# Performance work log

Measured on AMD Instinct MI355X. Metric: run time of the kernel, lower is better.

## Reference

```python
import jax, jax.numpy as jnp
import numpy as np

B, L, E, H = 2, 1024, 1024, 16
D = E // H  # head_dim = 64
EPS = 1e-6


def setup_inputs() -> dict:
    key = jax.random.key(0)
    ks = jax.random.split(key, 6)
    x = jax.random.normal(ks[0], (B, L, E), dtype=jnp.float32)
    qkv_w = jax.random.normal(ks[1], (E, 3 * E), dtype=jnp.float32) / np.sqrt(E)
    qkv_b = jnp.zeros((3 * E,), dtype=jnp.float32)
    out_w = jax.random.normal(ks[2], (E, E), dtype=jnp.float32) / np.sqrt(E)
    out_b = jnp.zeros((E,), dtype=jnp.float32)
    norm1_w = jnp.ones((E,), dtype=jnp.float32)
    norm2_w = jnp.ones((E,), dtype=jnp.float32)
    mlp_w1 = jax.random.normal(ks[3], (E, 4 * E), dtype=jnp.float32) / np.sqrt(E)
    mlp_b1 = jnp.zeros((4 * E,), dtype=jnp.float32)
    mlp_w2 = jax.random.normal(ks[4], (4 * E, E), dtype=jnp.float32) / np.sqrt(4 * E)
    mlp_b2 = jnp.zeros((E,), dtype=jnp.float32)
    return dict(x=x, qkv_w=qkv_w, qkv_b=qkv_b, out_w=out_w, out_b=out_b,
                norm1_w=norm1_w, norm2_w=norm2_w,
                mlp_w1=mlp_w1, mlp_b1=mlp_b1, mlp_w2=mlp_w2, mlp_b2=mlp_b2)


def rmsnorm(x, w, eps=1e-6):
    var = jnp.mean(jnp.square(x), axis=-1, keepdims=True)
    return x * jax.lax.rsqrt(var + eps) * w


def cosformer_attn(x, qkv_w, qkv_b, out_w, out_b):
    b, l, e = x.shape
    qkv = x @ qkv_w + qkv_b
    q, k, v = jnp.split(qkv, 3, axis=-1)
    # [B, H, L, D]
    q = q.reshape(b, l, H, D).transpose(0, 2, 1, 3)
    k = k.reshape(b, l, H, D).transpose(0, 2, 1, 3)
    v = v.reshape(b, l, H, D).transpose(0, 2, 1, 3)
    positions = jnp.arange(l, dtype=jnp.float32).reshape(1, 1, l, 1)
    cos_w = jnp.cos(jnp.pi / 2 * positions / l)
    sin_w = jnp.sin(jnp.pi / 2 * positions / l)
    q_prime = jax.nn.relu(q)
    k_prime = jax.nn.relu(k)
    q_cos, q_sin = q_prime * cos_w, q_prime * sin_w
    k_cos, k_sin = k_prime * cos_w, k_prime * sin_w
    # running KV state: cumsum over L of per-position outer products [B,H,L,D,D]
    kv_cos_cumsum = jnp.cumsum(jnp.einsum('bhld,bhle->bhlde', k_cos, v), axis=2)
    context_cos = jnp.einsum('bhld,bhlde->bhle', q_cos, kv_cos_cumsum)
    kv_sin_cumsum = jnp.cumsum(jnp.einsum('bhld,bhle->bhlde', k_sin, v), axis=2)
    context_sin = jnp.einsum('bhld,bhlde->bhle', q_sin, kv_sin_cumsum)
    context = context_cos + context_sin
    k_cos_cumsum = jnp.cumsum(k_cos, axis=2)
    k_sin_cumsum = jnp.cumsum(k_sin, axis=2)
    norm = (jnp.einsum('bhld,bhld->bhl', q_cos, k_cos_cumsum)
            + jnp.einsum('bhld,bhld->bhl', q_sin, k_sin_cumsum))
    output = context / (norm[..., None] + EPS)
    output = output.transpose(0, 2, 1, 3).reshape(b, l, e)
    return output @ out_w + out_b


def reference(x, qkv_w, qkv_b, out_w, out_b, norm1_w, norm2_w,
              mlp_w1, mlp_b1, mlp_w2, mlp_b2):
    # pre-norm transformer block with cosformer causal linear attention
    h = x + cosformer_attn(rmsnorm(x, norm1_w), qkv_w, qkv_b, out_w, out_b)
    m = rmsnorm(h, norm2_w)
    m = jax.nn.gelu(m @ mlp_w1 + mlp_b1) @ mlp_w2 + mlp_b2
    return h + m
```

## Files before the change

### kernel.cpp

```cpp
#include <hip/hip_runtime.h>

#define TB_L 1024
#define TB_E 1024

typedef __attribute__((ext_vector_type(8))) short bf16x8;
typedef __attribute__((ext_vector_type(8))) unsigned short u16x8;
typedef __attribute__((ext_vector_type(4))) float floatx4;

#define AS1(p) ((const __attribute__((address_space(1))) void*)(p))
#define AS3(p) ((__attribute__((address_space(3))) void*)(p))

static __device__ __forceinline__ unsigned short f2bf(float x) {
  union { float f; unsigned u; } c; c.f = x;
  unsigned r = c.u + 0x7fff + ((c.u >> 16) & 1);
  return (unsigned short)(r >> 16);
}
static __device__ __forceinline__ float gelu_f(float x) {
  const float c0 = 0.7978845608028654f;
  const float c1 = 0.044715f;
  float x3 = x * x * x;
  return 0.5f * x * (1.0f + tanhf(c0 * (x + c1 * x3)));
}

static __device__ __forceinline__ int swz(int row, int bytecol) {
  return row * 128 +
         ((((bytecol >> 4) ^ ((row + (row >> 3)) & 7)) << 4) | (bytecol & 15));
}

__global__ __launch_bounds__(256) void rms_kernel(const float* __restrict__ x,
                                                  const float* __restrict__ w,
                                                  unsigned short* __restrict__ out) {
  const int row = blockIdx.x;
  const int tid = threadIdx.x;
  const float4 v = *(const float4*)(x + (size_t)row * TB_E + tid * 4);
  float s = v.x * v.x + v.y * v.y + v.z * v.z + v.w * v.w;
#pragma unroll
  for (int off = 32; off > 0; off >>= 1) s += __shfl_down(s, off);
  __shared__ float red[4];
  if ((tid & 63) == 0) red[tid >> 6] = s;
  __syncthreads();
  const float tot = red[0] + red[1] + red[2] + red[3];
  const float scale = rsqrtf(tot * (1.0f / TB_E) + 1e-6f);
  const float4 wv = *(const float4*)(w + tid * 4);
  ushort4 o;
  o.x = f2bf(v.x * scale * wv.x);
  o.y = f2bf(v.y * scale * wv.y);
  o.z = f2bf(v.z * scale * wv.z);
  o.w = f2bf(v.w * scale * wv.w);
  *(ushort4*)(out + (size_t)row * TB_E + tid * 4) = o;
}

__global__ __launch_bounds__(256) void transpose_all(
    const float* __restrict__ s0, const float* __restrict__ s1,
    const float* __restrict__ s2, const float* __restrict__ s3,
    unsigned short* __restrict__ d0, unsigned short* __restrict__ d1,
    unsigned short* __restrict__ d2, unsigned short* __restrict__ d3) {
  const int id = blockIdx.x;
  const float* in; unsigned short* out; int K, N, lid;
  if (id < 768)       { in = s0; out = d0; K = 1024; N = 3072; lid = id; }
  else if (id < 1024) { in = s1; out = d1; K = 1024; N = 1024; lid = id - 768; }
  else if (id < 2048) { in = s2; out = d2; K = 1024; N = 4096; lid = id - 1024; }
  else                { in = s3; out = d3; K = 4096; N = 1024; lid = id - 2048; }
  const int nx = N >> 6;
  const int n0 = (lid % nx) * 64, k0 = (lid / nx) * 64;
  __shared__ float t[64][65];
  const int tid = threadIdx.x;
#pragma unroll
  for (int rep = 0; rep < 4; ++rep) {
    const int r = rep * 16 + (tid >> 4);
    const int c = (tid & 15) * 4;
    const float4 v = *(const float4*)(in + (size_t)(k0 + r) * N + n0 + c);
    t[r][c] = v.x; t[r][c + 1] = v.y; t[r][c + 2] = v.z; t[r][c + 3] = v.w;
  }
  __syncthreads();
#pragma unroll
  for (int rep = 0; rep < 4; ++rep) {
    const int n = rep * 16 + (tid >> 4);
    const int k = (tid & 15) * 4;
    ushort4 o;
    o.x = f2bf(t[k + 0][n]);
    o.y = f2bf(t[k + 1][n]);
    o.z = f2bf(t[k + 2][n]);
    o.w = f2bf(t[k + 3][n]);
    *(ushort4*)(out + (size_t)(n0 + n) * K + k0 + k) = o;
  }
}

template <int BM, int BN, int WM, int WN, bool GELU>
__global__ __launch_bounds__(256) void gemm_bf16(
    const unsigned short* __restrict__ A, const unsigned short* __restrict__ Bt,
    const float* __restrict__ bias, const float* __restrict__ res,
    float* __restrict__ Cf, unsigned short* __restrict__ Cb,
    float* __restrict__ Cpart, int M, int N, int K, int Ksl) {
  constexpr int WCOLS = BN / WN;
  constexpr int MT = WM / 16;
  constexpr int NT = WN / 16;
  constexpr int ACH = BM / 16;
  constexpr int BCH = BN / 16;
  static_assert((BM / WM) * (BN / WN) == 4, "4 waves");
  static_assert(ACH % 4 == 0 && BCH % 4 == 0, "chunks divisible by waves");
  __shared__ __align__(16) unsigned short As[2][BM * 32];
  __shared__ __align__(16) unsigned short Bs[2][BN * 32];
  const int tid = threadIdx.x;
  const int wid = tid >> 6, lane = tid & 63;
  const int m0 = blockIdx.y * BM, n0 = blockIdx.x * BN;
  const int k_off = blockIdx.z * Ksl;
  const int mbase = (wid / WCOLS) * WM, nbase = (wid % WCOLS) * WN;

  floatx4 acc[MT][NT];
#pragma unroll
  for (int i = 0; i < MT; ++i)
#pragma unroll
    for (int j = 0; j < NT; ++j) {
      floatx4 z = {0.f, 0.f, 0.f, 0.f};
      acc[i][j] = z;
    }

  const int srow = lane >> 2;
  const int scol = (lane & 3) * 8;
  const unsigned short* Ag = A + (size_t)m0 * K + k_off;
  const unsigned short* Bg = Bt + (size_t)n0 * K + k_off;
  const int fr = (lane & 15);
  const int fk = (lane >> 4) * 16;

  auto stage = [&](int buf, int k0) {
#pragma unroll
    for (int j = 0; j < ACH / 4; ++j) {
      const int ch = j * 4 + wid;
      __builtin_amdgcn_global_load_lds(
          AS1(Ag + (size_t)(ch * 16 + srow) * K + k0 + scol),
          AS3((char*)&As[buf][0] + ch * 1024), 16, 0, 0);
    }
#pragma unroll
    for (int j = 0; j < BCH / 4; ++j) {
      const int ch = j * 4 + wid;
      __builtin_amdgcn_global_load_lds(
          AS1(Bg + (size_t)(ch * 16 + srow) * K + k0 + scol),
          AS3((char*)&Bs[buf][0] + ch * 1024), 16, 0, 0);
    }
  };

  stage(0, 0);
  const int nsteps = Ksl / 32;
  for (int s = 0; s < nsteps; ++s) {
    __syncthreads();
    const int cur = s & 1;
    if (s + 1 < nsteps) stage(cur ^ 1, (s + 1) * 32);
    const char* Ab = (const char*)&As[cur][0];
    const char* Bb = (const char*)&Bs[cur][0];
    bf16x8 af[MT], bfr[NT];
#pragma unroll
    for (int i = 0; i < MT; ++i)
      af[i] = *(const bf16x8*)(Ab + (mbase / 16 + i) * 1024 + fr * 64 + fk);
#pragma unroll
    for (int j = 0; j < NT; ++j)
      bfr[j] = *(const bf16x8*)(Bb + (nbase / 16 + j) * 1024 + fr * 64 + fk);
#pragma unroll
    for (int i = 0; i < MT; ++i)
#pragma unroll
      for (int j = 0; j < NT; ++j)
        acc[i][j] = __builtin_amdgcn_mfma_f32_16x16x32_bf16(af[i], bfr[j],
                                                            acc[i][j], 0, 0, 0);
  }

  const int mr = (lane >> 4) * 4;
  const int nc = lane & 15;
  float* P = Cpart ? (Cpart + (size_t)blockIdx.z * M * N) : nullptr;
#pragma unroll
  for (int i = 0; i < MT; ++i)
#pragma unroll
    for (int j = 0; j < NT; ++j) {
      const int n = n0 + nbase + j * 16 + nc;
      const float bv = bias ? bias[n] : 0.f;
#pragma unroll
      for (int r = 0; r < 4; ++r) {
        const int m = m0 + mbase + i * 16 + mr + r;
        float v = acc[i][j][r] + bv;
        if (GELU) v = gelu_f(v);
        if (res) v += res[(size_t)m * N + n];
        if (P) P[(size_t)m * N + n] = v;
        if (Cf) Cf[(size_t)m * N + n] = v;
        if (Cb) Cb[(size_t)m * N + n] = f2bf(v);
      }
    }
}

__global__ __launch_bounds__(256) void reduce_out(const float* __restrict__ P,
                                                  const float* __restrict__ h,
                                                  const float* __restrict__ b2,
                                                  float* __restrict__ out) {
  const int idx = (blockIdx.x * 256 + threadIdx.x) * 4;
  const int n = idx & 1023;
  const float4 a = *(const float4*)(P + idx);
  const float4 b = *(const float4*)(P + 2097152 + idx);
  const float4 hh = *(const float4*)(h + idx);
  const float4 bb = *(const float4*)(b2 + n);
  float4 o;
  o.x = a.x + b.x + hh.x + bb.x;
  o.y = a.y + b.y + hh.y + bb.y;
  o.z = a.z + b.z + hh.z + bb.z;
  o.w = a.w + b.w + hh.w + bb.w;
  *(float4*)(out + idx) = o;
}

__global__ __launch_bounds__(256) void attn_mfma(const unsigned short* __restrict__ qkv,
                                                 unsigned short* __restrict__ out) {
  const int it = blockIdx.x;
  const int bh = blockIdx.y;
  const int b = bh >> 4, h = bh & 15;
  const int tid = threadIdx.x;
  const int w = tid >> 6, lane = tid & 63;
  const int qd = lane >> 4, ln = lane & 15;
  const int i0 = it * 64;
  __shared__ __align__(16) char sq[8192];
  __shared__ __align__(16) char sk[8192];
  __shared__ __align__(16) char svt[8192];
  __shared__ __align__(16) char ss[8192];
  const unsigned short* base = qkv + (size_t)b * (TB_L * 3072) + h * 64;
  const float PH = 1.5339807878856412e-3f;

#pragma unroll
  for (int p = 0; p < 2; ++p) {
    const int flat = p * 256 + tid;
    const int r = flat >> 3, c = flat & 7;
    u16x8 v = *(const u16x8*)(base + (size_t)(i0 + r) * 3072 + c * 8);
#pragma unroll
    for (int z = 0; z < 8; ++z) v[z] = (v[z] & 0x8000) ? (unsigned short)0 : v[z];
    *(u16x8*)(sq + swz(r, c * 16)) = v;
  }
  __syncthreads();

  bf16x8 aq[2];
#pragma unroll
  for (int ks = 0; ks < 2; ++ks)
    aq[ks] = *(const bf16x8*)(sq + swz(w * 16 + ln, ks * 64 + qd * 16));

  float ci[4], si[4];
#pragma unroll
  for (int r = 0; r < 4; ++r)
    __sincosf(PH * (float)(i0 + w * 16 + qd * 4 + r), &si[r], &ci[r]);

  floatx4 acc_o[4], acc_n;
  {
    floatx4 z = {0.f, 0.f, 0.f, 0.f};
#pragma unroll
    for (int nt = 0; nt < 4; ++nt) acc_o[nt] = z;
    acc_n = z;
  }
  bf16x8 ones;
#pragma unroll
  for (int z = 0; z < 8; ++z) ones[z] = (short)0x3F80;

  for (int jt = 0; jt <= it; ++jt) {
    const int j0 = jt * 64;
    __syncthreads();
#pragma unroll
    for (int p = 0; p < 2; ++p) {
      const int flat = p * 256 + tid;
      const int r = flat >> 3, c = flat & 7;
      u16x8 kv = *(const u16x8*)(base + (size_t)(j0 + r) * 3072 + 1024 + c * 8);
#pragma unroll
      for (int z = 0; z < 8; ++z) kv[z] = (kv[z] & 0x8000) ? (unsigned short)0 : kv[z];
      *(u16x8*)(sk + swz(r, c * 16)) = kv;
      u16x8 vv = *(const u16x8*)(base + (size_t)(j0 + r) * 3072 + 2048 + c * 8);
#pragma unroll
      for (int z = 0; z < 8; ++z)
        *(unsigned short*)(svt + swz(c * 8 + z, r * 2)) = (unsigned short)vv[z];
    }
    __syncthreads();

    floatx4 s_acc[4];
    {
      floatx4 z = {0.f, 0.f, 0.f, 0.f};
#pragma unroll
      for (int nt = 0; nt < 4; ++nt) s_acc[nt] = z;
    }
#pragma unroll
    for (int ks = 0; ks < 2; ++ks)
#pragma unroll
      for (int nt = 0; nt < 4; ++nt) {
        const bf16x8 bk = *(const bf16x8*)(sk + swz(nt * 16 + ln, ks * 64 + qd * 16));
        s_acc[nt] = __builtin_amdgcn_mfma_f32_16x16x32_bf16(aq[ks], bk, s_acc[nt], 0, 0, 0);
      }

    float cj[4], sj[4];
#pragma unroll
    for (int nt = 0; nt < 4; ++nt)
      __sincosf(PH * (float)(j0 + nt * 16 + ln), &sj[nt], &cj[nt]);
    const bool diag = (jt == it);
    const int li = w * 16 + qd * 4;
#pragma unroll
    for (int nt = 0; nt < 4; ++nt) {
      const int jl = nt * 16 + ln;
#pragma unroll
      for (int r = 0; r < 4; ++r) {
        float val = s_acc[nt][r] * (ci[r] * cj[nt] + si[r] * sj[nt]);
        if (diag && jl > li + r) val = 0.f;
        *(unsigned short*)(ss + swz(li + r, jl * 2)) = f2bf(val);
      }
    }

#pragma unroll
    for (int ks = 0; ks < 2; ++ks) {
      const bf16x8 as = *(const bf16x8*)(ss + swz(w * 16 + ln, ks * 64 + qd * 16));
#pragma unroll
      for (int nt = 0; nt < 4; ++nt) {
        const bf16x8 bv = *(const bf16x8*)(svt + swz(nt * 16 + ln, ks * 64 + qd * 16));
        acc_o[nt] = __builtin_amdgcn_mfma_f32_16x16x32_bf16(as, bv, acc_o[nt], 0, 0, 0);
      }
      acc_n = __builtin_amdgcn_mfma_f32_16x16x32_bf16(as, ones, acc_n, 0, 0, 0);
    }
  }

#pragma unroll
  for (int r = 0; r < 4; ++r) {
    const float inv = 1.0f / (acc_n[r] + 1e-6f);
    unsigned short* op =
        out + (size_t)(b * TB_L + i0 + w * 16 + qd * 4 + r) * TB_E + h * 64;
#pragma unroll
    for (int nt = 0; nt < 4; ++nt) op[nt * 16 + ln] = f2bf(acc_o[nt][r] * inv);
  }
}

extern "C" void kernel_launch(void* const* d_in, const int* in_sizes, int n_in,
                              void* d_out, int out_size, void* d_ws, size_t ws_size,
                              hipStream_t stream) {
  const float* x     = (const float*)d_in[0];
  const float* qkv_w = (const float*)d_in[1];
  const float* qkv_b = (const float*)d_in[2];
  const float* out_w = (const float*)d_in[3];
  const float* out_b = (const float*)d_in[4];
  const float* n1w   = (const float*)d_in[5];
  const float* n2w   = (const float*)d_in[6];
  const float* w1    = (const float*)d_in[7];
  const float* b1    = (const float*)d_in[8];
  const float* w2    = (const float*)d_in[9];
  const float* b2    = (const float*)d_in[10];

  char* wsb = (char*)d_ws;
  unsigned short* qkvb  = (unsigned short*)wsb;
  unsigned short* g     = (unsigned short*)wsb;
  unsigned short* xnb   = (unsigned short*)(wsb + 16777216);
  unsigned short* attnb = (unsigned short*)(wsb + 20971520);
  float*          h     = (float*)(wsb + 25165824);
  unsigned short* qkvwt = (unsigned short*)(wsb + 33554432);
  unsigned short* outwt = (unsigned short*)(wsb + 39845888);
  unsigned short* w1t   = (unsigned short*)(wsb + 41943040);
  unsigned short* w2t   = (unsigned short*)(wsb + 50331648);
  float*          Pk    = (float*)(wsb + 33554432);
  float* out = (float*)d_out;
  const int M = 2048;

  transpose_all<<<dim3(3072), 256, 0, stream>>>(qkv_w, out_w, w1, w2,
                                                qkvwt, outwt, w1t, w2t);

  rms_kernel<<<dim3(M), 256, 0, stream>>>(x, n1w, xnb);
  gemm_bf16<64, 128, 32, 64, false><<<dim3(24, 32), 256, 0, stream>>>(
      xnb, qkvwt, qkv_b, nullptr, nullptr, qkvb, nullptr, M, 3072, 1024, 1024);
  attn_mfma<<<dim3(16, 32), 256, 0, stream>>>(qkvb, attnb);
  gemm_bf16<64, 64, 32, 32, false><<<dim3(16, 32), 256, 0, stream>>>(
      attnb, outwt, out_b, x, h, nullptr, nullptr, M, 1024, 1024, 1024);
  rms_kernel<<<dim3(M), 256, 0, stream>>>(h, n2w, xnb);
  gemm_bf16<64, 128, 32, 64, true><<<dim3(32, 32), 256, 0, stream>>>(
      xnb, w1t, b1, nullptr, nullptr, g, nullptr, M, 4096, 1024, 1024);
  gemm_bf16<64, 64, 32, 32, false><<<dim3(16, 32, 2), 256, 0, stream>>>(
      g, w2t, nullptr, nullptr, nullptr, nullptr, Pk, M, 1024, 4096, 2048);
  reduce_out<<<dim3(2048), 256, 0, stream>>>(Pk, h, b2, out);
}
```

Measured before the change: 279.0 us.

## Generalize GEMM to BK=64 and 8-wave blocks with grouped tile rasterization

Parameterizes the bf16 GEMM on K-tile depth and thread count, doubling K per stage to 64 so each barrier covers two MFMA k-chunks. The large GEMMs now use 512-thread blocks with 32x32 per-wave tiles, and the second MLP GEMM moves to 64x128 tiles. It also adds grouped block rasterization (groups of 4 M-tiles) to improve L2 reuse of the weight tiles. This doubles LDS use per block and changes the register and occupancy balance.

After: 264.8 us. -5.1%, faster.

```diff
diff --git a/kernel.cpp b/kernel.cpp
--- a/kernel.cpp
+++ b/kernel.cpp
@@ -86,24 +86,33 @@
   }
 }
 
-template <int BM, int BN, int WM, int WN, bool GELU>
-__global__ __launch_bounds__(256) void gemm_bf16(
+template <int BM, int BN, int BK, int WM, int WN, int NTH, bool GELU>
+__global__ __launch_bounds__(NTH) void gemm_bf16(
     const unsigned short* __restrict__ A, const unsigned short* __restrict__ Bt,
     const float* __restrict__ bias, const float* __restrict__ res,
     float* __restrict__ Cf, unsigned short* __restrict__ Cb,
     float* __restrict__ Cpart, int M, int N, int K, int Ksl) {
+  constexpr int NW = NTH / 64;
+  constexpr int KC = BK / 32;
   constexpr int WCOLS = BN / WN;
   constexpr int MT = WM / 16;
   constexpr int NT = WN / 16;
-  constexpr int ACH = BM / 16;
-  constexpr int BCH = BN / 16;
-  static_assert((BM / WM) * (BN / WN) == 4, "4 waves");
-  static_assert(ACH % 4 == 0 && BCH % 4 == 0, "chunks divisible by waves");
-  __shared__ __align__(16) unsigned short As[2][BM * 32];
-  __shared__ __align__(16) unsigned short Bs[2][BN * 32];
+  constexpr int ACH = (BM / 16) * KC;
+  constexpr int BCH = (BN / 16) * KC;
+  static_assert((BM / WM) * (BN / WN) == NW, "wave grid");
+  static_assert(ACH % NW == 0 && BCH % NW == 0, "chunks divisible by waves");
+  __shared__ __align__(16) unsigned short As[2][BM * BK];
+  __shared__ __align__(16) unsigned short Bs[2][BN * BK];
   const int tid = threadIdx.x;
   const int wid = tid >> 6, lane = tid & 63;
-  const int m0 = blockIdx.y * BM, n0 = blockIdx.x * BN;
+
+  constexpr int G = 4;
+  const int nbx = gridDim.x;
+  const int flat = blockIdx.y * nbx + blockIdx.x;
+  const int grp = flat / (G * nbx), rem = flat % (G * nbx);
+  const int m0 = (grp * G + rem % G) * BM;
+  const int n0 = (rem / G) * BN;
+
   const int k_off = blockIdx.z * Ksl;
   const int mbase = (wid / WCOLS) * WM, nbase = (wid % WCOLS) * WN;
 
@@ -125,42 +134,49 @@
 
   auto stage = [&](int buf, int k0) {
 #pragma unroll
-    for (int j = 0; j < ACH / 4; ++j) {
-      const int ch = j * 4 + wid;
+    for (int j = 0; j < ACH / NW; ++j) {
+      const int ch = j * NW + wid;
+      const int strip = ch / KC, half = ch % KC;
       __builtin_amdgcn_global_load_lds(
-          AS1(Ag + (size_t)(ch * 16 + srow) * K + k0 + scol),
+          AS1(Ag + (size_t)(strip * 16 + srow) * K + k0 + half * 32 + scol),
           AS3((char*)&As[buf][0] + ch * 1024), 16, 0, 0);
     }
 #pragma unroll
-    for (int j = 0; j < BCH / 4; ++j) {
-      const int ch = j * 4 + wid;
+    for (int j = 0; j < BCH / NW; ++j) {
+      const int ch = j * NW + wid;
+      const int strip = ch / KC, half = ch % KC;
       __builtin_amdgcn_global_load_lds(
-          AS1(Bg + (size_t)(ch * 16 + srow) * K + k0 + scol),
+          AS1(Bg + (size_t)(strip * 16 + srow) * K + k0 + half * 32 + scol),
           AS3((char*)&Bs[buf][0] + ch * 1024), 16, 0, 0);
     }
   };
 
   stage(0, 0);
-  const int nsteps = Ksl / 32;
+  const int nsteps = Ksl / BK;
   for (int s = 0; s < nsteps; ++s) {
     __syncthreads();
     const int cur = s & 1;
-    if (s + 1 < nsteps) stage(cur ^ 1, (s + 1) * 32);
+    if (s + 1 < nsteps) stage(cur ^ 1, (s + 1) * BK);
     const char* Ab = (const char*)&As[cur][0];
     const char* Bb = (const char*)&Bs[cur][0];
-    bf16x8 af[MT], bfr[NT];
-#pragma unroll
-    for (int i = 0; i < MT; ++i)
-      af[i] = *(const bf16x8*)(Ab + (mbase / 16 + i) * 1024 + fr * 64 + fk);
-#pragma unroll
-    for (int j = 0; j < NT; ++j)
-      bfr[j] = *(const bf16x8*)(Bb + (nbase / 16 + j) * 1024 + fr * 64 + fk);
-#pragma unroll
-    for (int i = 0; i < MT; ++i)
+#pragma unroll
+    for (int g = 0; g < KC; ++g) {
+      bf16x8 af[MT], bfr[NT];
+#pragma unroll
+      for (int i = 0; i < MT; ++i)
+        af[i] = *(const bf16x8*)(Ab + ((mbase / 16 + i) * KC + g) * 1024 +
+                                 fr * 64 + fk);
 #pragma unroll
       for (int j = 0; j < NT; ++j)
-        acc[i][j] = __builtin_amdgcn_mfma_f32_16x16x32_bf16(af[i], bfr[j],
-                                                            acc[i][j], 0, 0, 0);
+        bfr[j] = *(const bf16x8*)(Bb + ((nbase / 16 + j) * KC + g) * 1024 +
+                                  fr * 64 + fk);
+#pragma unroll
+      for (int i = 0; i < MT; ++i)
+#pragma unroll
+        for (int j = 0; j < NT; ++j)
+          acc[i][j] = __builtin_amdgcn_mfma_f32_16x16x32_bf16(af[i], bfr[j],
+                                                              acc[i][j], 0, 0, 0);
+    }
   }
 
   const int mr = (lane >> 4) * 4;
@@ -355,15 +371,15 @@
                                                 qkvwt, outwt, w1t, w2t);
 
   rms_kernel<<<dim3(M), 256, 0, stream>>>(x, n1w, xnb);
-  gemm_bf16<64, 128, 32, 64, false><<<dim3(24, 32), 256, 0, stream>>>(
+  gemm_bf16<64, 128, 64, 32, 32, 512, false><<<dim3(24, 32), 512, 0, stream>>>(
       xnb, qkvwt, qkv_b, nullptr, nullptr, qkvb, nullptr, M, 3072, 1024, 1024);
   attn_mfma<<<dim3(16, 32), 256, 0, stream>>>(qkvb, attnb);
-  gemm_bf16<64, 64, 32, 32, false><<<dim3(16, 32), 256, 0, stream>>>(
+  gemm_bf16<64, 64, 64, 32, 32, 256, false><<<dim3(16, 32), 256, 0, stream>>>(
       attnb, outwt, out_b, x, h, nullptr, nullptr, M, 1024, 1024, 1024);
   rms_kernel<<<dim3(M), 256, 0, stream>>>(h, n2w, xnb);
-  gemm_bf16<64, 128, 32, 64, true><<<dim3(32, 32), 256, 0, stream>>>(
+  gemm_bf16<64, 128, 64, 32, 32, 512, true><<<dim3(32, 32), 512, 0, stream>>>(
       xnb, w1t, b1, nullptr, nullptr, g, nullptr, M, 4096, 1024, 1024);
-  gemm_bf16<64, 64, 32, 32, false><<<dim3(16, 32, 2), 256, 0, stream>>>(
+  gemm_bf16<64, 128, 64, 32, 32, 512, false><<<dim3(8, 32, 2), 512, 0, stream>>>(
       g, w2t, nullptr, nullptr, nullptr, nullptr, Pk, M, 1024, 4096, 2048);
   reduce_out<<<dim3(2048), 256, 0, stream>>>(Pk, h, b2, out);
 }
```
